# Kernel optimization log

Measured on AMD Instinct MI355X. Metric: run time of the kernel, lower is better.

## Reference

```python
import jax, jax.numpy as jnp
import numpy as np

EOS_IDX = 1
B, S, V, E, H = 32, 64, 32000, 512, 512


def _gru_step(x, h, w_ih, w_hh, b_ih, b_hh):
    # PyTorch GRU cell: gates ordered (r, z, n)
    gi = x @ w_ih.T + b_ih
    gh = h @ w_hh.T + b_hh
    i_r, i_z, i_n = jnp.split(gi, 3, axis=-1)
    h_r, h_z, h_n = jnp.split(gh, 3, axis=-1)
    r = jax.nn.sigmoid(i_r + h_r)
    z = jax.nn.sigmoid(i_z + h_z)
    n = jnp.tanh(i_n + r * h_n)
    return (1.0 - z) * n + z * h


def setup_inputs() -> dict:
    key = jax.random.key(0)
    ks = jax.random.split(key, 16)
    u = lambda k, shape: jax.random.uniform(k, shape, jnp.float32, -1.0, 1.0) / np.sqrt(H)
    return {
        "targets": jax.random.randint(ks[0], (B, S), 0, V),
        "targets_kws": jax.random.randint(ks[1], (B, S), 0, V),
        "sent_state": jax.random.normal(ks[2], (1, B, H), jnp.float32),
        "targets_len": jax.random.randint(ks[3], (B,), 1, S),
        "emb": jax.random.normal(ks[4], (V, E), jnp.float32) * 0.05,
        "w_ih_w": u(ks[5], (3 * H, 2 * E)),
        "w_hh_w": u(ks[6], (3 * H, H)),
        "b_ih_w": u(ks[7], (3 * H,)),
        "b_hh_w": u(ks[8], (3 * H,)),
        "w_ih_s": u(ks[9], (3 * H, H)),
        "w_hh_s": u(ks[10], (3 * H, H)),
        "b_ih_s": u(ks[11], (3 * H,)),
        "b_hh_s": u(ks[12], (3 * H,)),
        "out_w": u(ks[13], (V, H)),
        "out_b": u(ks[14], (V,)),
    }


def reference(targets, targets_kws, sent_state, targets_len,
              emb, w_ih_w, w_hh_w, b_ih_w, b_hh_w,
              w_ih_s, w_hh_s, b_ih_s, b_hh_s, out_w, out_b):
    seq = targets.shape[1]
    h0 = sent_state[0]  # nlayers = 1 -> (B, H)
    last_words = targets[:, :-1].T   # (S-1, B)
    keywords = targets_kws[:, 1:].T  # (S-1, B)
    next_words = targets[:, 1:].T    # (S-1, B)

    def step(carry, inp):
        word_h, sent_h = carry
        lw, kw, nw = inp
        x = jnp.concatenate([emb[kw], emb[lw]], axis=-1)  # (B, 2E)
        word_h = _gru_step(x, word_h, w_ih_w, w_hh_w, b_ih_w, b_hh_w)
        logp = jax.nn.log_softmax(word_h @ out_w.T + out_b, axis=-1)
        m = (nw == EOS_IDX).astype(word_h.dtype)[:, None]  # EOS mask
        tmp = _gru_step(word_h, sent_h, w_ih_s, w_hh_s, b_ih_s, b_hh_s)
        sent_h2 = sent_h * (1.0 - m) + tmp * m
        word_h2 = word_h * (1.0 - m) + tmp * m
        return (word_h2, sent_h2), logp

    _, logps = jax.lax.scan(step, (h0, h0), (last_words, keywords, next_words))
    # logps: (S-1, B, V). Masked NLL as in mask_loss().
    tok_logp = jnp.take_along_axis(logps, next_words[:, :, None], axis=2)[:, :, 0]
    valid = (targets_len[None, :] > jnp.arange(1, seq)[:, None]).astype(logps.dtype)
    return -(tok_logp * valid).sum()
```

## Files before the change

kernel.cpp:

```cpp
#include <hip/hip_runtime.h>
#include <stdint.h>

typedef short bf16x8 __attribute__((ext_vector_type(8)));
typedef float f32x4 __attribute__((ext_vector_type(4)));
typedef unsigned short u16;
typedef unsigned long long u64;

#define B_  32
#define S_  64
#define V_  32000
#define H_  512
#define T_  63
#define R_  2016
#define RP_ 2048
#define G3_ 1536
#define NWG 32
#define NWORK 192

#define o_X      0ull
#define o_Wih    4194304ull
#define o_OutW   7340032ull
#define o_PackHH 40108032ull
#define o_PackIS 41680896ull
#define o_PackHS 43253760ull
#define o_GI     44826624ull
#define o_WHf    57212928ull
#define o_WHb    61341696ull
#define o_HPUB   63438848ull
#define o_SPUB   63504384ull
#define o_ARR    63569920ull
#define o_CTR    63571968ull
#define o_PART   63733760ull
#define o_LSE    72122368ull
#define o_RL     72130560ull
#define o_FLG    72138752ull
#define o_HFLG   72139776ull

__device__ __forceinline__ u16 f2b(float f) {
  unsigned u = __float_as_uint(f);
  u = (u + 0x7FFFu + ((u >> 16) & 1u)) >> 16;
  return (u16)u;
}
__device__ __forceinline__ float sigm(float x) { return 1.0f / (1.0f + __expf(-x)); }

__device__ __forceinline__ void fbar(int* arr, int ph, int tid) {
  __syncthreads();
  if (tid == 0) {
    __hip_atomic_fetch_add(&arr[ph], 1, __ATOMIC_RELAXED, __HIP_MEMORY_SCOPE_AGENT);
    while (__hip_atomic_load(&arr[ph], __ATOMIC_RELAXED, __HIP_MEMORY_SCOPE_AGENT) < NWG)
      __builtin_amdgcn_s_sleep(1);
  }
  __syncthreads();
}

__global__ __launch_bounds__(256) void k_cvt(const float* __restrict__ src,
                                             u16* __restrict__ dst, int n) {
  int i4 = (blockIdx.x * 256 + threadIdx.x) * 4;
  if (i4 < n) {
    float4 v = *(const float4*)(src + i4);
    u16 t[4] = {f2b(v.x), f2b(v.y), f2b(v.z), f2b(v.w)};
    *(uint2*)(dst + i4) = *(uint2*)t;
  }
}

__global__ __launch_bounds__(256) void k_pack(const float* __restrict__ w, u16* __restrict__ up) {
  int uid = blockIdx.x * 256 + threadIdx.x;
  int lane = uid & 63;
  int ksct = uid >> 6;
  int ks = ksct & 15, ct = ksct >> 4;
  int nrow = ct * 16 + (lane & 15);
  int k0 = ks * 32 + (lane >> 4) * 8;
  const float* p = w + (size_t)nrow * 512 + k0;
  float4 v0 = *(const float4*)p;
  float4 v1 = *(const float4*)(p + 4);
  u16 t[8] = {f2b(v0.x), f2b(v0.y), f2b(v0.z), f2b(v0.w),
              f2b(v1.x), f2b(v1.y), f2b(v1.z), f2b(v1.w)};
  *(uint4*)(up + (size_t)uid * 8) = *(uint4*)t;
}

__global__ __launch_bounds__(256) void k_gather(const float* __restrict__ emb,
                                                const int* __restrict__ tg,
                                                const int* __restrict__ tk,
                                                u16* __restrict__ X) {
  int r = blockIdx.x;
  int tid = threadIdx.x;
  u16* xr = X + (size_t)r * 1024;
  if (r < R_) {
    int t = r >> 5, b = r & 31;
    int kw = tk[b * 64 + t + 1];
    int lw = tg[b * 64 + t];
    const float* src = (tid < 128) ? (emb + (size_t)kw * 512 + tid * 4)
                                   : (emb + (size_t)lw * 512 + (tid - 128) * 4);
    float4 v = *(const float4*)src;
    u16 o[4] = {f2b(v.x), f2b(v.y), f2b(v.z), f2b(v.w)};
    *(uint2*)(xr + tid * 4) = *(uint2*)o;
  } else {
    u16 z[4] = {0, 0, 0, 0};
    *(uint2*)(xr + tid * 4) = *(uint2*)z;
  }
}

__global__ __launch_bounds__(256) void k_init(const float* __restrict__ sent,
                                              const int* __restrict__ tg,
                                              u64* __restrict__ hpub, u64* __restrict__ spub,
                                              u16* __restrict__ whb, int* __restrict__ flg,
                                              int* __restrict__ arr, int* __restrict__ ctr,
                                              int* __restrict__ hflg) {
  int idx = blockIdx.x * 256 + threadIdx.x;
  whb[(size_t)R_ * 512 + idx] = 0;
  if (idx < 2048) {
    int b = idx >> 6, c = idx & 63;
    const float* p = sent + (size_t)b * 512 + c * 8;
    float4 v0 = *(const float4*)p;
    float4 v1 = *(const float4*)(p + 4);
    u16 t[8] = {f2b(v0.x), f2b(v0.y), f2b(v0.z), f2b(v0.w),
                f2b(v1.x), f2b(v1.y), f2b(v1.z), f2b(v1.w)};
    int slot = c ^ (b & 7);
    u64* d = hpub + b * 128 + slot * 2;
    d[0] = ((const u64*)t)[0];
    d[1] = ((const u64*)t)[1];
    u64* s = spub + b * 128 + slot * 2;
    s[0] = ((const u64*)t)[0];
    s[1] = ((const u64*)t)[1];
  }
  if (blockIdx.x == 0 && threadIdx.x < 63) {
    int f = 0;
    for (int b = 0; b < 32; ++b) f |= (tg[b * 64 + threadIdx.x + 1] == 1);
    flg[threadIdx.x] = f;
  }
  if (blockIdx.x == 1) arr[threadIdx.x] = 0;
  if (blockIdx.x == 2) ctr[threadIdx.x] = 0;
  if (blockIdx.x == 3) hflg[threadIdx.x] = 0;
  if (blockIdx.x == 4) hflg[256 + threadIdx.x] = 0;
}

__global__ __launch_bounds__(256) void k_gemm0(const u16* __restrict__ A, const u16* __restrict__ Bw,
                                               const float* __restrict__ bias, int N, int K, int nrt,
                                               float* __restrict__ outC, int Mstore) {
  __shared__ u16 As[128 * 64];
  __shared__ u16 Bs[128 * 64];
  int bid = blockIdx.x;
  int rt = bid % nrt, ct = bid / nrt;
  int m0 = rt * 128, n0 = ct * 128;
  int tid = threadIdx.x;
  int lane = tid & 63, wid = tid >> 6;
  int wr = wid >> 1, wc = wid & 1;
  f32x4 z = {0.f, 0.f, 0.f, 0.f};
  f32x4 acc[4][4];
#pragma unroll
  for (int i = 0; i < 4; ++i)
#pragma unroll
    for (int j = 0; j < 4; ++j) acc[i][j] = z;

  int nkt = K >> 6;
  for (int kt = 0; kt < nkt; ++kt) {
    __syncthreads();
#pragma unroll
    for (int it = 0; it < 4; ++it) {
      int idx = it * 256 + tid;
      int row = idx >> 3;
      int kch = idx & 7;
      int sch = kch ^ (row & 7);
      *(uint4*)(&As[row * 64 + kch * 8]) =
          *(const uint4*)(A + (size_t)(m0 + row) * K + kt * 64 + sch * 8);
      *(uint4*)(&Bs[row * 64 + kch * 8]) =
          *(const uint4*)(Bw + (size_t)(n0 + row) * K + kt * 64 + sch * 8);
    }
    __syncthreads();
#pragma unroll
    for (int kk = 0; kk < 2; ++kk) {
      bf16x8 af[4], bf[4];
#pragma unroll
      for (int i = 0; i < 4; ++i) {
        int row = wr * 64 + i * 16 + (lane & 15);
        int c = kk * 4 + (lane >> 4);
        af[i] = *(const bf16x8*)(&As[row * 64 + ((c ^ (row & 7)) * 8)]);
      }
#pragma unroll
      for (int j = 0; j < 4; ++j) {
        int row = wc * 64 + j * 16 + (lane & 15);
        int c = kk * 4 + (lane >> 4);
        bf[j] = *(const bf16x8*)(&Bs[row * 64 + ((c ^ (row & 7)) * 8)]);
      }
#pragma unroll
      for (int i = 0; i < 4; ++i)
#pragma unroll
        for (int j = 0; j < 4; ++j)
          acc[i][j] = __builtin_amdgcn_mfma_f32_16x16x32_bf16(af[i], bf[j], acc[i][j], 0, 0, 0);
    }
  }
#pragma unroll
  for (int i = 0; i < 4; ++i) {
    int mb = m0 + wr * 64 + i * 16 + ((lane >> 4) << 2);
#pragma unroll
    for (int j = 0; j < 4; ++j) {
      int n = n0 + wc * 64 + j * 16 + (lane & 15);
      float bb = bias[n];
#pragma unroll
      for (int r = 0; r < 4; ++r) {
        int m = mb + r;
        if (m < Mstore) outC[(size_t)m * N + n] = acc[i][j][r] + bb;
      }
    }
  }
}

struct RecurSM {
  u16 hb[32 * 512];
  u16 wls[3 * 1024 * 8];
  float ghl[6][32][16];
  float gil[2][3][32][16];
  float hloc[32][16];
  float sloc[32][16];
  u16 hps[32][16];
  u16 sps[32][16];
};
struct GemmSM {
  u16 As[128 * 64];
  u16 Bs[128 * 64];
};
union MegaSM {
  RecurSM r;
  GemmSM g;
};

__device__ __forceinline__ f32x4 mm16_lds(const u16* hb, const u16* bl, int lane, int rt) {
  f32x4 a0 = {0.f, 0.f, 0.f, 0.f}, a1 = {0.f, 0.f, 0.f, 0.f};
  int row = rt * 16 + (lane & 15);
  int cb = lane >> 4;
#pragma unroll
  for (int ks = 0; ks < 16; ks += 2) {
    int c0 = ks * 4 + cb, c1 = c0 + 4;
    bf16x8 av0 = *(const bf16x8*)(&hb[row * 512 + ((c0 ^ (row & 7)) * 8)]);
    bf16x8 bv0 = *(const bf16x8*)(&bl[(ks * 64 + lane) * 8]);
    bf16x8 av1 = *(const bf16x8*)(&hb[row * 512 + ((c1 ^ (row & 7)) * 8)]);
    bf16x8 bv1 = *(const bf16x8*)(&bl[((ks + 1) * 64 + lane) * 8]);
    a0 = __builtin_amdgcn_mfma_f32_16x16x32_bf16(av0, bv0, a0, 0, 0, 0);
    a1 = __builtin_amdgcn_mfma_f32_16x16x32_bf16(av1, bv1, a1, 0, 0, 0);
  }
  return a0 + a1;
}

__device__ __forceinline__ f32x4 mm16g(const u16* hb, const u16* bp, int lane, int rt) {
  f32x4 acc = {0.f, 0.f, 0.f, 0.f};
#pragma unroll
  for (int ks = 0; ks < 16; ++ks) {
    int row = rt * 16 + (lane & 15);
    int c = ks * 4 + (lane >> 4);
    bf16x8 a = *(const bf16x8*)(&hb[row * 512 + ((c ^ (row & 7)) * 8)]);
    bf16x8 b = *(const bf16x8*)(bp + (size_t)(ks * 64 + lane) * 8);
    acc = __builtin_amdgcn_mfma_f32_16x16x32_bf16(a, b, acc, 0, 0, 0);
  }
  return acc;
}

__device__ __forceinline__ void gemm_tile(u16* As, u16* Bs, const u16* __restrict__ A,
                                          const u16* __restrict__ Bw,
                                          const float* __restrict__ bias,
                                          int rt, int ct, float2* __restrict__ parts, int tid) {
  int m0 = rt * 128, n0 = ct * 128;
  int lane = tid & 63, wid = tid >> 6;
  int wr = wid >> 1, wc = wid & 1;
  f32x4 z = {0.f, 0.f, 0.f, 0.f};
  f32x4 acc[2][4];
#pragma unroll
  for (int i = 0; i < 2; ++i)
#pragma unroll
    for (int j = 0; j < 4; ++j) acc[i][j] = z;

  for (int kt = 0; kt < 8; ++kt) {
    __syncthreads();
#pragma unroll
    for (int it = 0; it < 2; ++it) {
      int idx = it * 512 + tid;
      int row = idx >> 3, kch = idx & 7;
      *(uint4*)(&As[row * 64 + kch * 8]) =
          *(const uint4*)(A + (size_t)(m0 + row) * 512 + kt * 64 + kch * 8);
      int sch = kch ^ (row & 7);
      *(uint4*)(&Bs[row * 64 + kch * 8]) =
          *(const uint4*)(Bw + (size_t)(n0 + row) * 512 + kt * 64 + sch * 8);
    }
    __syncthreads();
#pragma unroll
    for (int kk = 0; kk < 2; ++kk) {
      bf16x8 af[2], bf[4];
#pragma unroll
      for (int i = 0; i < 2; ++i) {
        int row = wr * 32 + i * 16 + (lane & 15);
        int c = kk * 4 + (lane >> 4);
        af[i] = *(const bf16x8*)(&As[row * 64 + ((c ^ (row & 7)) * 8)]);
      }
#pragma unroll
      for (int j = 0; j < 4; ++j) {
        int row = wc * 64 + j * 16 + (lane & 15);
        int c = kk * 4 + (lane >> 4);
        bf[j] = *(const bf16x8*)(&Bs[row * 64 + ((c ^ (row & 7)) * 8)]);
      }
#pragma unroll
      for (int i = 0; i < 2; ++i)
#pragma unroll
        for (int j = 0; j < 4; ++j)
          acc[i][j] = __builtin_amdgcn_mfma_f32_16x16x32_bf16(af[i], bf[j], acc[i][j], 0, 0, 0);
    }
  }
  float bb[4];
#pragma unroll
  for (int j = 0; j < 4; ++j) bb[j] = bias[n0 + wc * 64 + j * 16 + (lane & 15)];
  int chunk = ct * 2 + wc;
#pragma unroll
  for (int i = 0; i < 2; ++i) {
#pragma unroll
    for (int r = 0; r < 4; ++r) {
      float l0 = acc[i][0][r] + bb[0], l1 = acc[i][1][r] + bb[1];
      float l2 = acc[i][2][r] + bb[2], l3 = acc[i][3][r] + bb[3];
      float mx = fmaxf(fmaxf(l0, l1), fmaxf(l2, l3));
#pragma unroll
      for (int d = 1; d < 16; d <<= 1) mx = fmaxf(mx, __shfl_xor(mx, d));
      float s = __expf(l0 - mx) + __expf(l1 - mx) + __expf(l2 - mx) + __expf(l3 - mx);
#pragma unroll
      for (int d = 1; d < 16; d <<= 1) s += __shfl_xor(s, d);
      if ((lane & 15) == 0) {
        int m = m0 + wr * 32 + i * 16 + ((lane >> 4) << 2) + r;
        parts[(size_t)m * 512 + chunk] = make_float2(mx, s);
      }
    }
  }
}

__global__ __launch_bounds__(512) void k_mega(
    const float* __restrict__ gi, const u16* __restrict__ packHH, const u16* __restrict__ packIS,
    const u16* __restrict__ packHS, const float* __restrict__ bhh_w, const float* __restrict__ bih_s,
    const float* __restrict__ bhh_s, const int* __restrict__ targets, const int* __restrict__ flags,
    const float* __restrict__ sent, u64* __restrict__ hpub, u64* __restrict__ spub,
    float* __restrict__ whf, u16* __restrict__ whb, int* __restrict__ arr, int* __restrict__ ctr,
    int* __restrict__ hflg, u16* __restrict__ outw16, const float* __restrict__ outw,
    const float* __restrict__ outb, float2* __restrict__ parts) {
  __shared__ MegaSM sm;
  const int tid = threadIdx.x;
  int* steps = ctr + 32;

  if (blockIdx.x >= NWG) {
    const int w = blockIdx.x - NWG;
    const int nown = (w < 58) ? 2 : 1;
#pragma unroll
    for (int p = 0; p < 2; ++p) {
      if (p < nown) {
        int ct = w + p * 192;
        const float* src = outw + (size_t)ct * 65536;
        u16* dst = outw16 + (size_t)ct * 65536;
        for (int it = 0; it < 32; ++it) {
          int e = it * 512 + tid;
          float4 v = *(const float4*)(src + (size_t)e * 4);
          u16 t[4] = {f2b(v.x), f2b(v.y), f2b(v.z), f2b(v.w)};
          *(uint2*)(dst + (size_t)e * 4) = *(uint2*)t;
        }
      }
    }
    __syncthreads();
    for (int rt = 0; rt < 16; ++rt) {
      if (tid == 0) {
        int need = 4 * rt + 4;
        if (need > T_) need = T_;
        while (__hip_atomic_load(steps, __ATOMIC_RELAXED, __HIP_MEMORY_SCOPE_AGENT) < need)
          __builtin_amdgcn_s_sleep(64);
        (void)__hip_atomic_load(steps, __ATOMIC_ACQUIRE, __HIP_MEMORY_SCOPE_AGENT);
      }
      for (int p = 0; p < nown; ++p)
        gemm_tile(sm.g.As, sm.g.Bs, whb, outw16, outb, rt, w + p * 192, parts, tid);
      __syncthreads();
    }
    return;
  }

  const int lane = tid & 63;
  const int wid = tid >> 6;
  const int gate = wid >> 1;
  const int rt = wid & 1;
  const int g = blockIdx.x;
  const int b_ = tid >> 4, hl = tid & 15;
  const int n_ = g * 16 + hl;

  {
    const uint4* src = (const uint4*)packHH;
    uint4* dst = (uint4*)sm.r.wls;
    for (int lin = tid; lin < 3072; lin += 512) {
      int which = lin >> 10, off = lin & 1023;
      dst[lin] = src[(size_t)(which * 32 + g) * 1024 + off];
    }
  }
  {
    float v = sent[(size_t)b_ * 512 + n_];
    sm.r.hloc[b_][hl] = v;
    sm.r.sloc[b_][hl] = v;
  }
  if (wid >= 6) {
    int lid = tid - 384;
    const float* base = gi + (size_t)g * 16;
#pragma unroll
    for (int q = 0; q < 3; ++q) {
      int fid = q * 128 + lid;
      int ga = fid >> 7, rem = fid & 127;
      int b = rem >> 2, h4 = (rem & 3) << 2;
      *(float4*)&sm.r.gil[0][ga][b][h4] = *(const float4*)(base + (size_t)b * 1536 + ga * 512 + h4);
    }
  }
  const float bw_r = bhh_w[n_], bw_z = bhh_w[512 + n_], bw_n = bhh_w[1024 + n_];
  __syncthreads();

  int ph = 0;
  int scur = 0;
  for (int t = 0; t < T_; ++t) {
    const int cur = t & 1, nxt = cur ^ 1;
    if (wid == 0) {
      for (;;) {
        int f = (lane < 32)
            ? __hip_atomic_load(&hflg[lane * 16], __ATOMIC_RELAXED, __HIP_MEMORY_SCOPE_AGENT)
            : 0x7fffffff;
        if (__all(f >= t)) break;
        __builtin_amdgcn_s_sleep(1);
      }
      if (g == 0 && lane == 0)
        __hip_atomic_store(steps, t, __ATOMIC_RELEASE, __HIP_MEMORY_SCOPE_AGENT);
    }
    __syncthreads();
    {
      const u64* src = hpub + cur * 4096;
      u64* d = (u64*)sm.r.hb;
      for (int idx = tid; idx < 4096; idx += 512)
        d[idx] = __hip_atomic_load(&src[idx], __ATOMIC_RELAXED, __HIP_MEMORY_SCOPE_AGENT);
    }
    __syncthreads();
    if (wid < 6) {
      f32x4 acc = mm16_lds(sm.r.hb, sm.r.wls + gate * 8192, lane, rt);
      int bb = rt * 16 + ((lane >> 4) << 2);
      int cl = lane & 15;
#pragma unroll
      for (int r4 = 0; r4 < 4; ++r4) sm.r.ghl[gate][bb + r4][cl] = acc[r4];
    } else if (t + 1 < T_) {
      int lid = tid - 384;
      const float* base = gi + (size_t)(t + 1) * 32 * 1536 + g * 16;
#pragma unroll
      for (int q = 0; q < 3; ++q) {
        int fid = q * 128 + lid;
        int ga = fid >> 7, rem = fid & 127;
        int b = rem >> 2, h4 = (rem & 3) << 2;
        *(float4*)&sm.r.gil[nxt][ga][b][h4] =
            *(const float4*)(base + (size_t)b * 1536 + ga * 512 + h4);
      }
    }
    __syncthreads();
    {
      int rrow = t * 32 + b_;
      float r_ = sigm(sm.r.gil[cur][0][b_][hl] + sm.r.ghl[0][b_][hl] + bw_r);
      float z_ = sigm(sm.r.gil[cur][1][b_][hl] + sm.r.ghl[1][b_][hl] + bw_z);
      float nn = tanhf(sm.r.gil[cur][2][b_][hl] + r_ * (sm.r.ghl[2][b_][hl] + bw_n));
      float hold = sm.r.hloc[b_][hl];
      float hnew = (1.f - z_) * nn + z_ * hold;
      sm.r.hloc[b_][hl] = hnew;
      sm.r.hps[b_][hl] = f2b(hnew);
      whf[(size_t)rrow * 512 + n_] = hnew;
    }
    __syncthreads();
    if (tid < 128) {
      int b = tid >> 2, j = tid & 3, q = j >> 1, half = j & 1;
      u64 v = *(const u64*)&sm.r.hps[b][q * 8 + half * 4];
      int slot = (2 * g + q) ^ (b & 7);
      __hip_atomic_store(&hpub[nxt * 4096 + b * 128 + slot * 2 + half], v,
                         __ATOMIC_RELAXED, __HIP_MEMORY_SCOPE_AGENT);
    } else if (tid < 256) {
      int l = tid - 128;
      int b = l >> 2, j = l & 3, q = j >> 1, half = j & 1;
      u64 v = *(const u64*)&sm.r.hps[b][q * 8 + half * 4];
      int slot = (2 * g + q) ^ (b & 7);
      __hip_atomic_store((u64*)whb + (size_t)(t * 32 + b) * 128 + slot * 2 + half, v,
                         __ATOMIC_RELAXED, __HIP_MEMORY_SCOPE_AGENT);
    }

    if (!flags[t]) {
      __syncthreads();
      if (tid == 0)
        __hip_atomic_store(&hflg[g * 16], t + 1, __ATOMIC_RELAXED, __HIP_MEMORY_SCOPE_AGENT);
    } else {
      fbar(arr, ph, tid); ++ph;
      {
        const u64* src = hpub + nxt * 4096;
        u64* d = (u64*)sm.r.hb;
        for (int idx = tid; idx < 4096; idx += 512)
          d[idx] = __hip_atomic_load(&src[idx], __ATOMIC_RELAXED, __HIP_MEMORY_SCOPE_AGENT);
      }
      fbar(arr, ph, tid); ++ph;
      f32x4 ax = {0.f, 0.f, 0.f, 0.f};
      if (wid < 6) ax = mm16g(sm.r.hb, packIS + (size_t)(gate * 32 + g) * 8192, lane, rt);
      __syncthreads();
      {
        const u64* src = spub + scur * 4096;
        u64* d = (u64*)sm.r.hb;
        for (int idx = tid; idx < 4096; idx += 512)
          d[idx] = __hip_atomic_load(&src[idx], __ATOMIC_RELAXED, __HIP_MEMORY_SCOPE_AGENT);
      }
      __syncthreads();
      if (wid < 6) {
        f32x4 ah = mm16g(sm.r.hb, packHS + (size_t)(gate * 32 + g) * 8192, lane, rt);
        int bb = rt * 16 + ((lane >> 4) << 2);
        int cl = lane & 15;
#pragma unroll
        for (int r4 = 0; r4 < 4; ++r4) {
          sm.r.ghl[gate][bb + r4][cl] = ax[r4];
          sm.r.ghl[3 + gate][bb + r4][cl] = ah[r4];
        }
      }
      __syncthreads();
      {
        float r_ = sigm(sm.r.ghl[0][b_][hl] + bih_s[n_] + sm.r.ghl[3][b_][hl] + bhh_s[n_]);
        float z_ = sigm(sm.r.ghl[1][b_][hl] + bih_s[512 + n_] + sm.r.ghl[4][b_][hl] + bhh_s[512 + n_]);
        float nn = tanhf(sm.r.ghl[2][b_][hl] + bih_s[1024 + n_] +
                         r_ * (sm.r.ghl[5][b_][hl] + bhh_s[1024 + n_]));
        float hs = sm.r.sloc[b_][hl];
        float tmpv = (1.f - z_) * nn + z_ * hs;
        int m = (targets[b_ * 64 + t + 1] == 1);
        float hw = sm.r.hloc[b_][hl];
        float hw2 = m ? tmpv : hw;
        float hs2 = m ? tmpv : hs;
        sm.r.hloc[b_][hl] = hw2;
        sm.r.sloc[b_][hl] = hs2;
        sm.r.hps[b_][hl] = f2b(hw2);
        sm.r.sps[b_][hl] = f2b(hs2);
      }
      __syncthreads();
      if (tid < 128) {
        int b = tid >> 2, j = tid & 3, q = j >> 1, half = j & 1;
        int slot = (2 * g + q) ^ (b & 7);
        u64 v = *(const u64*)&sm.r.hps[b][q * 8 + half * 4];
        __hip_atomic_store(&hpub[nxt * 4096 + b * 128 + slot * 2 + half], v,
                           __ATOMIC_RELAXED, __HIP_MEMORY_SCOPE_AGENT);
        u64 w2 = *(const u64*)&sm.r.sps[b][q * 8 + half * 4];
        __hip_atomic_store(&spub[(scur ^ 1) * 4096 + b * 128 + slot * 2 + half], w2,
                           __ATOMIC_RELAXED, __HIP_MEMORY_SCOPE_AGENT);
      }
      scur ^= 1;
      __syncthreads();
      if (tid == 0)
        __hip_atomic_store(&hflg[g * 16], t + 1, __ATOMIC_RELAXED, __HIP_MEMORY_SCOPE_AGENT);
    }
  }
  if (g == 0 && wid == 0) {
    for (;;) {
      int f = (lane < 32)
          ? __hip_atomic_load(&hflg[lane * 16], __ATOMIC_RELAXED, __HIP_MEMORY_SCOPE_AGENT)
          : 0x7fffffff;
      if (__all(f >= T_)) break;
      __builtin_amdgcn_s_sleep(1);
    }
    if (lane == 0)
      __hip_atomic_store(steps, T_, __ATOMIC_RELEASE, __HIP_MEMORY_SCOPE_AGENT);
  }
}

__global__ __launch_bounds__(256) void k_lse(const float2* __restrict__ parts,
                                             float* __restrict__ lse) {
  int wid = threadIdx.x >> 6, lane = threadIdx.x & 63;
  int row = blockIdx.x * 4 + wid;
  if (row >= R_) return;
  float m = -3.0e38f, s = 0.f;
  for (int c = lane; c < 500; c += 64) {
    float2 p = parts[(size_t)row * 512 + c];
    float nm = fmaxf(m, p.x);
    s = s * __expf(m - nm) + p.y * __expf(p.x - nm);
    m = nm;
  }
#pragma unroll
  for (int d = 1; d < 64; d <<= 1) {
    float om = __shfl_xor(m, d), os = __shfl_xor(s, d);
    float nm = fmaxf(m, om);
    s = s * __expf(m - nm) + os * __expf(om - nm);
    m = nm;
  }
  if (lane == 0) lse[row] = m + __logf(s);
}

__global__ __launch_bounds__(256) void k_rowloss(const float* __restrict__ whf,
                                                 const float* __restrict__ outw,
                                                 const float* __restrict__ outb,
                                                 const int* __restrict__ targets,
                                                 const int* __restrict__ tlen,
                                                 const float* __restrict__ lse,
                                                 float* __restrict__ rl) {
  int wid = threadIdx.x >> 6, lane = threadIdx.x & 63;
  int r = blockIdx.x * 4 + wid;
  if (r >= R_) return;
  int t = r >> 5, b = r & 31;
  int nw = targets[b * 64 + t + 1];
  const float* hv = whf + (size_t)r * 512;
  const float* wv = outw + (size_t)nw * 512;
  float acc = 0.f;
#pragma unroll
  for (int q = 0; q < 2; ++q) {
    int k = lane * 8 + q * 4;
    float4 a = *(const float4*)(hv + k);
    float4 w = *(const float4*)(wv + k);
    acc += a.x * w.x + a.y * w.y + a.z * w.z + a.w * w.w;
  }
#pragma unroll
  for (int d = 1; d < 64; d <<= 1) acc += __shfl_xor(acc, d);
  if (lane == 0) {
    bool valid = tlen[b] > (t + 1);
    rl[r] = valid ? (lse[r] - (acc + outb[nw])) : 0.f;
  }
}

__global__ __launch_bounds__(256) void k_sum(const float* __restrict__ rl, float* __restrict__ out) {
  __shared__ float sm[256];
  float a = 0.f;
  for (int i = threadIdx.x; i < R_; i += 256) a += rl[i];
  sm[threadIdx.x] = a;
  __syncthreads();
  for (int s = 128; s > 0; s >>= 1) {
    if (threadIdx.x < s) sm[threadIdx.x] += sm[threadIdx.x + s];
    __syncthreads();
  }
  if (threadIdx.x == 0) out[0] = sm[0];
}

extern "C" void kernel_launch(void* const* d_in, const int* in_sizes, int n_in,
                              void* d_out, int out_size, void* d_ws, size_t ws_size,
                              hipStream_t stream) {
  const int* targets = (const int*)d_in[0];
  const int* tkws    = (const int*)d_in[1];
  const float* sent  = (const float*)d_in[2];
  const int* tlen    = (const int*)d_in[3];
  const float* emb   = (const float*)d_in[4];
  const float* wihw  = (const float*)d_in[5];
  const float* whhw  = (const float*)d_in[6];
  const float* bihw  = (const float*)d_in[7];
  const float* bhhw  = (const float*)d_in[8];
  const float* wihs  = (const float*)d_in[9];
  const float* whhs  = (const float*)d_in[10];
  const float* bihs  = (const float*)d_in[11];
  const float* bhhs  = (const float*)d_in[12];
  const float* outw  = (const float*)d_in[13];
  const float* outb  = (const float*)d_in[14];
  float* out = (float*)d_out;
  char* ws = (char*)d_ws;

  u16* X       = (u16*)(ws + o_X);
  u16* Wih16   = (u16*)(ws + o_Wih);
  u16* OutW16  = (u16*)(ws + o_OutW);
  u16* PackHH  = (u16*)(ws + o_PackHH);
  u16* PackIS  = (u16*)(ws + o_PackIS);
  u16* PackHS  = (u16*)(ws + o_PackHS);
  float* GI    = (float*)(ws + o_GI);
  float* WHf   = (float*)(ws + o_WHf);
  u16* WHb     = (u16*)(ws + o_WHb);
  u64* HPUB    = (u64*)(ws + o_HPUB);
  u64* SPUB    = (u64*)(ws + o_SPUB);
  int* ARR     = (int*)(ws + o_ARR);
  int* CTR     = (int*)(ws + o_CTR);
  float2* PART = (float2*)(ws + o_PART);
  float* LSE   = (float*)(ws + o_LSE);
  float* RL    = (float*)(ws + o_RL);
  int* FLG     = (int*)(ws + o_FLG);
  int* HFLG    = (int*)(ws + o_HFLG);

  k_cvt<<<dim3(1536), dim3(256), 0, stream>>>(wihw, Wih16, G3_ * 1024);
  k_pack<<<dim3(384), dim3(256), 0, stream>>>(whhw, PackHH);
  k_pack<<<dim3(384), dim3(256), 0, stream>>>(wihs, PackIS);
  k_pack<<<dim3(384), dim3(256), 0, stream>>>(whhs, PackHS);
  k_gather<<<dim3(RP_), dim3(256), 0, stream>>>(emb, targets, tkws, X);
  k_init<<<dim3(64), dim3(256), 0, stream>>>(sent, targets, HPUB, SPUB, WHb, FLG, ARR, CTR, HFLG);

  k_gemm0<<<dim3(16 * 12), dim3(256), 0, stream>>>(X, Wih16, bihw, G3_, 1024, 16, GI, R_);

  k_mega<<<dim3(NWG + NWORK), dim3(512), 0, stream>>>(GI, PackHH, PackIS, PackHS, bhhw, bihs, bhhs,
                                                      targets, FLG, sent, HPUB, SPUB, WHf, WHb,
                                                      ARR, CTR, HFLG, OutW16, outw, outb, PART);

  k_lse<<<dim3(504), dim3(256), 0, stream>>>(PART, LSE);
  k_rowloss<<<dim3(504), dim3(256), 0, stream>>>(WHf, outw, outb, targets, tlen, LSE, RL);
  k_sum<<<dim3(1), dim3(256), 0, stream>>>(RL, out);
}
```

Before: 393.6 us.

## Fuse prep kernels into one launch, fuse LSE/rowloss/sum, shrink worker grid

Merges the six preprocessing kernels (convert, three packs, gather, init) into a single k_prep launch dispatched by block index. It also merges the log-sum-exp, row-loss and final-sum kernels into one k_final that reduces per timestep and adds into the output with atomicAdd. The output is zeroed in k_prep. Separately, the number of output-GEMM worker blocks in the persistent kernel drops from 192 to 128, so more workers own two column tiles. This cuts launch overhead and intermediate buffers, but the smaller worker count may lengthen the logits GEMM tail, and the float atomic sum makes the result order-dependent.

```diff
diff --git a/kernel.cpp b/kernel.cpp
--- a/kernel.cpp
+++ b/kernel.cpp
@@ -15,7 +15,7 @@
 #define RP_ 2048
 #define G3_ 1536
 #define NWG 32
-#define NWORK 192
+#define NWORK 128
 
 #define o_X      0ull
 #define o_Wih    4194304ull
@@ -53,85 +53,89 @@
   __syncthreads();
 }
 
-__global__ __launch_bounds__(256) void k_cvt(const float* __restrict__ src,
-                                             u16* __restrict__ dst, int n) {
-  int i4 = (blockIdx.x * 256 + threadIdx.x) * 4;
-  if (i4 < n) {
-    float4 v = *(const float4*)(src + i4);
-    u16 t[4] = {f2b(v.x), f2b(v.y), f2b(v.z), f2b(v.w)};
-    *(uint2*)(dst + i4) = *(uint2*)t;
-  }
-}
-
-__global__ __launch_bounds__(256) void k_pack(const float* __restrict__ w, u16* __restrict__ up) {
-  int uid = blockIdx.x * 256 + threadIdx.x;
-  int lane = uid & 63;
-  int ksct = uid >> 6;
-  int ks = ksct & 15, ct = ksct >> 4;
-  int nrow = ct * 16 + (lane & 15);
-  int k0 = ks * 32 + (lane >> 4) * 8;
-  const float* p = w + (size_t)nrow * 512 + k0;
-  float4 v0 = *(const float4*)p;
-  float4 v1 = *(const float4*)(p + 4);
-  u16 t[8] = {f2b(v0.x), f2b(v0.y), f2b(v0.z), f2b(v0.w),
-              f2b(v1.x), f2b(v1.y), f2b(v1.z), f2b(v1.w)};
-  *(uint4*)(up + (size_t)uid * 8) = *(uint4*)t;
-}
-
-__global__ __launch_bounds__(256) void k_gather(const float* __restrict__ emb,
-                                                const int* __restrict__ tg,
-                                                const int* __restrict__ tk,
-                                                u16* __restrict__ X) {
-  int r = blockIdx.x;
-  int tid = threadIdx.x;
-  u16* xr = X + (size_t)r * 1024;
-  if (r < R_) {
-    int t = r >> 5, b = r & 31;
-    int kw = tk[b * 64 + t + 1];
-    int lw = tg[b * 64 + t];
-    const float* src = (tid < 128) ? (emb + (size_t)kw * 512 + tid * 4)
-                                   : (emb + (size_t)lw * 512 + (tid - 128) * 4);
-    float4 v = *(const float4*)src;
-    u16 o[4] = {f2b(v.x), f2b(v.y), f2b(v.z), f2b(v.w)};
-    *(uint2*)(xr + tid * 4) = *(uint2*)o;
+__global__ __launch_bounds__(256) void k_prep(
+    const float* __restrict__ emb, const int* __restrict__ tg, const int* __restrict__ tk,
+    u16* __restrict__ X, const float* __restrict__ sent, u64* __restrict__ hpub,
+    u64* __restrict__ spub, u16* __restrict__ whb, int* __restrict__ flg, int* __restrict__ arr,
+    int* __restrict__ ctr, int* __restrict__ hflg, const float* __restrict__ wihw,
+    u16* __restrict__ wih16, const float* __restrict__ whhw, u16* __restrict__ packHH,
+    const float* __restrict__ wihs, u16* __restrict__ packIS, const float* __restrict__ whhs,
+    u16* __restrict__ packHS, float* __restrict__ out) {
+  const int bid = blockIdx.x;
+  const int tid = threadIdx.x;
+  if (bid < 2048) {
+    int r = bid;
+    u16* xr = X + (size_t)r * 1024;
+    if (r < R_) {
+      int t = r >> 5, b = r & 31;
+      int kw = tk[b * 64 + t + 1];
+      int lw = tg[b * 64 + t];
+      const float* src = (tid < 128) ? (emb + (size_t)kw * 512 + tid * 4)
+                                     : (emb + (size_t)lw * 512 + (tid - 128) * 4);
+      float4 v = *(const float4*)src;
+      u16 o[4] = {f2b(v.x), f2b(v.y), f2b(v.z), f2b(v.w)};
+      *(uint2*)(xr + tid * 4) = *(uint2*)o;
+    } else {
+      u16 z[4] = {0, 0, 0, 0};
+      *(uint2*)(xr + tid * 4) = *(uint2*)z;
+    }
+  } else if (bid < 2112) {
+    int lb = bid - 2048;
+    int idx = lb * 256 + tid;
+    whb[(size_t)R_ * 512 + idx] = 0;
+    if (idx < 2048) {
+      int b = idx >> 6, c = idx & 63;
+      const float* p = sent + (size_t)b * 512 + c * 8;
+      float4 v0 = *(const float4*)p;
+      float4 v1 = *(const float4*)(p + 4);
+      u16 t[8] = {f2b(v0.x), f2b(v0.y), f2b(v0.z), f2b(v0.w),
+                  f2b(v1.x), f2b(v1.y), f2b(v1.z), f2b(v1.w)};
+      int slot = c ^ (b & 7);
+      u64* d = hpub + b * 128 + slot * 2;
+      d[0] = ((const u64*)t)[0];
+      d[1] = ((const u64*)t)[1];
+      u64* s = spub + b * 128 + slot * 2;
+      s[0] = ((const u64*)t)[0];
+      s[1] = ((const u64*)t)[1];
+    }
+    if (lb == 0 && tid < 63) {
+      int f = 0;
+      for (int b = 0; b < 32; ++b) f |= (tg[b * 64 + tid + 1] == 1);
+      flg[tid] = f;
+    }
+    if (lb == 1) arr[tid] = 0;
+    if (lb == 2) ctr[tid] = 0;
+    if (lb == 3) hflg[tid] = 0;
+    if (lb == 4) hflg[256 + tid] = 0;
+    if (lb == 5 && tid == 0) out[0] = 0.f;
+  } else if (bid < 3648) {
+    int i4 = ((bid - 2112) * 256 + tid) * 4;
+    if (i4 < G3_ * 1024) {
+      float4 v = *(const float4*)(wihw + i4);
+      u16 t[4] = {f2b(v.x), f2b(v.y), f2b(v.z), f2b(v.w)};
+      *(uint2*)(wih16 + i4) = *(uint2*)t;
+    }
   } else {
-    u16 z[4] = {0, 0, 0, 0};
-    *(uint2*)(xr + tid * 4) = *(uint2*)z;
-  }
-}
-
-__global__ __launch_bounds__(256) void k_init(const float* __restrict__ sent,
-                                              const int* __restrict__ tg,
-                                              u64* __restrict__ hpub, u64* __restrict__ spub,
-                                              u16* __restrict__ whb, int* __restrict__ flg,
-                                              int* __restrict__ arr, int* __restrict__ ctr,
-                                              int* __restrict__ hflg) {
-  int idx = blockIdx.x * 256 + threadIdx.x;
-  whb[(size_t)R_ * 512 + idx] = 0;
-  if (idx < 2048) {
-    int b = idx >> 6, c = idx & 63;
-    const float* p = sent + (size_t)b * 512 + c * 8;
+    int pb = bid - 3648;
+    const float* w;
+    u16* up;
+    int lb;
+    if (pb < 384) { w = whhw; up = packHH; lb = pb; }
+    else if (pb < 768) { w = wihs; up = packIS; lb = pb - 384; }
+    else { w = whhs; up = packHS; lb = pb - 768; }
+    int uid = lb * 256 + tid;
+    int lane = uid & 63;
+    int ksct = uid >> 6;
+    int ks = ksct & 15, ct = ksct >> 4;
+    int nrow = ct * 16 + (lane & 15);
+    int k0 = ks * 32 + (lane >> 4) * 8;
+    const float* p = w + (size_t)nrow * 512 + k0;
     float4 v0 = *(const float4*)p;
     float4 v1 = *(const float4*)(p + 4);
     u16 t[8] = {f2b(v0.x), f2b(v0.y), f2b(v0.z), f2b(v0.w),
                 f2b(v1.x), f2b(v1.y), f2b(v1.z), f2b(v1.w)};
-    int slot = c ^ (b & 7);
-    u64* d = hpub + b * 128 + slot * 2;
-    d[0] = ((const u64*)t)[0];
-    d[1] = ((const u64*)t)[1];
-    u64* s = spub + b * 128 + slot * 2;
-    s[0] = ((const u64*)t)[0];
-    s[1] = ((const u64*)t)[1];
-  }
-  if (blockIdx.x == 0 && threadIdx.x < 63) {
-    int f = 0;
-    for (int b = 0; b < 32; ++b) f |= (tg[b * 64 + threadIdx.x + 1] == 1);
-    flg[threadIdx.x] = f;
-  }
-  if (blockIdx.x == 1) arr[threadIdx.x] = 0;
-  if (blockIdx.x == 2) ctr[threadIdx.x] = 0;
-  if (blockIdx.x == 3) hflg[threadIdx.x] = 0;
-  if (blockIdx.x == 4) hflg[256 + threadIdx.x] = 0;
+    *(uint4*)(up + (size_t)uid * 8) = *(uint4*)t;
+  }
 }
 
 __global__ __launch_bounds__(256) void k_gemm0(const u16* __restrict__ A, const u16* __restrict__ Bw,
@@ -341,11 +345,11 @@
 
   if (blockIdx.x >= NWG) {
     const int w = blockIdx.x - NWG;
-    const int nown = (w < 58) ? 2 : 1;
+    const int nown = (w < 122) ? 2 : 1;
 #pragma unroll
     for (int p = 0; p < 2; ++p) {
       if (p < nown) {
-        int ct = w + p * 192;
+        int ct = w + p * NWORK;
         const float* src = outw + (size_t)ct * 65536;
         u16* dst = outw16 + (size_t)ct * 65536;
         for (int it = 0; it < 32; ++it) {
@@ -366,7 +370,7 @@
         (void)__hip_atomic_load(steps, __ATOMIC_ACQUIRE, __HIP_MEMORY_SCOPE_AGENT);
       }
       for (int p = 0; p < nown; ++p)
-        gemm_tile(sm.g.As, sm.g.Bs, whb, outw16, outb, rt, w + p * 192, parts, tid);
+        gemm_tile(sm.g.As, sm.g.Bs, whb, outw16, outb, rt, w + p * NWORK, parts, tid);
       __syncthreads();
     }
     return;
@@ -556,69 +560,62 @@
   }
 }
 
-__global__ __launch_bounds__(256) void k_lse(const float2* __restrict__ parts,
-                                             float* __restrict__ lse) {
-  int wid = threadIdx.x >> 6, lane = threadIdx.x & 63;
-  int row = blockIdx.x * 4 + wid;
-  if (row >= R_) return;
-  float m = -3.0e38f, s = 0.f;
-  for (int c = lane; c < 500; c += 64) {
-    float2 p = parts[(size_t)row * 512 + c];
-    float nm = fmaxf(m, p.x);
-    s = s * __expf(m - nm) + p.y * __expf(p.x - nm);
-    m = nm;
-  }
-#pragma unroll
-  for (int d = 1; d < 64; d <<= 1) {
-    float om = __shfl_xor(m, d), os = __shfl_xor(s, d);
-    float nm = fmaxf(m, om);
-    s = s * __expf(m - nm) + os * __expf(om - nm);
-    m = nm;
-  }
-  if (lane == 0) lse[row] = m + __logf(s);
-}
-
-__global__ __launch_bounds__(256) void k_rowloss(const float* __restrict__ whf,
-                                                 const float* __restrict__ outw,
-                                                 const float* __restrict__ outb,
-                                                 const int* __restrict__ targets,
-                                                 const int* __restrict__ tlen,
-                                                 const float* __restrict__ lse,
-                                                 float* __restrict__ rl) {
-  int wid = threadIdx.x >> 6, lane = threadIdx.x & 63;
-  int r = blockIdx.x * 4 + wid;
-  if (r >= R_) return;
-  int t = r >> 5, b = r & 31;
-  int nw = targets[b * 64 + t + 1];
-  const float* hv = whf + (size_t)r * 512;
-  const float* wv = outw + (size_t)nw * 512;
-  float acc = 0.f;
-#pragma unroll
-  for (int q = 0; q < 2; ++q) {
-    int k = lane * 8 + q * 4;
-    float4 a = *(const float4*)(hv + k);
-    float4 w = *(const float4*)(wv + k);
-    acc += a.x * w.x + a.y * w.y + a.z * w.z + a.w * w.w;
-  }
-#pragma unroll
-  for (int d = 1; d < 64; d <<= 1) acc += __shfl_xor(acc, d);
-  if (lane == 0) {
-    bool valid = tlen[b] > (t + 1);
-    rl[r] = valid ? (lse[r] - (acc + outb[nw])) : 0.f;
-  }
-}
-
-__global__ __launch_bounds__(256) void k_sum(const float* __restrict__ rl, float* __restrict__ out) {
-  __shared__ float sm[256];
-  float a = 0.f;
-  for (int i = threadIdx.x; i < R_; i += 256) a += rl[i];
-  sm[threadIdx.x] = a;
+__global__ __launch_bounds__(512) void k_final(const float2* __restrict__ parts,
+                                               const float* __restrict__ whf,
+                                               const float* __restrict__ outw,
+                                               const float* __restrict__ outb,
+                                               const int* __restrict__ targets,
+                                               const int* __restrict__ tlen,
+                                               float* __restrict__ out) {
+  const int t = blockIdx.x;
+  const int tid = threadIdx.x;
+  const int wv = tid >> 6, lane = tid & 63;
+  __shared__ float wsum[8];
+  float lsum = 0.f;
+#pragma unroll
+  for (int q = 0; q < 4; ++q) {
+    int b = wv * 4 + q;
+    int r = t * 32 + b;
+    float m = -3.0e38f, s = 0.f;
+    for (int c = lane; c < 500; c += 64) {
+      float2 p = parts[(size_t)r * 512 + c];
+      float nm = fmaxf(m, p.x);
+      s = s * __expf(m - nm) + p.y * __expf(p.x - nm);
+      m = nm;
+    }
+#pragma unroll
+    for (int d = 1; d < 64; d <<= 1) {
+      float om = __shfl_xor(m, d), os = __shfl_xor(s, d);
+      float nm = fmaxf(m, om);
+      s = s * __expf(m - nm) + os * __expf(om - nm);
+      m = nm;
+    }
+    float lse = m + __logf(s);
+    int nw = targets[b * 64 + t + 1];
+    const float* hv = whf + (size_t)r * 512;
+    const float* wvp = outw + (size_t)nw * 512;
+    int k = lane * 8;
+    float4 a0 = *(const float4*)(hv + k);
+    float4 w0 = *(const float4*)(wvp + k);
+    float4 a1 = *(const float4*)(hv + k + 4);
+    float4 w1 = *(const float4*)(wvp + k + 4);
+    float acc = a0.x * w0.x + a0.y * w0.y + a0.z * w0.z + a0.w * w0.w +
+                a1.x * w1.x + a1.y * w1.y + a1.z * w1.z + a1.w * w1.w;
+#pragma unroll
+    for (int d = 1; d < 64; d <<= 1) acc += __shfl_xor(acc, d);
+    if (lane == 0) {
+      bool valid = tlen[b] > (t + 1);
+      lsum += valid ? (lse - (acc + outb[nw])) : 0.f;
+    }
+  }
+  if (lane == 0) wsum[wv] = lsum;
   __syncthreads();
-  for (int s = 128; s > 0; s >>= 1) {
-    if (threadIdx.x < s) sm[threadIdx.x] += sm[threadIdx.x + s];
-    __syncthreads();
-  }
-  if (threadIdx.x == 0) out[0] = sm[0];
+  if (tid == 0) {
+    float a = 0.f;
+#pragma unroll
+    for (int i = 0; i < 8; ++i) a += wsum[i];
+    atomicAdd(out, a);
+  }
 }
 
 extern "C" void kernel_launch(void* const* d_in, const int* in_sizes, int n_in,
@@ -656,17 +653,12 @@
   int* ARR     = (int*)(ws + o_ARR);
   int* CTR     = (int*)(ws + o_CTR);
   float2* PART = (float2*)(ws + o_PART);
-  float* LSE   = (float*)(ws + o_LSE);
-  float* RL    = (float*)(ws + o_RL);
   int* FLG     = (int*)(ws + o_FLG);
   int* HFLG    = (int*)(ws + o_HFLG);
 
-  k_cvt<<<dim3(1536), dim3(256), 0, stream>>>(wihw, Wih16, G3_ * 1024);
-  k_pack<<<dim3(384), dim3(256), 0, stream>>>(whhw, PackHH);
-  k_pack<<<dim3(384), dim3(256), 0, stream>>>(wihs, PackIS);
-  k_pack<<<dim3(384), dim3(256), 0, stream>>>(whhs, PackHS);
-  k_gather<<<dim3(RP_), dim3(256), 0, stream>>>(emb, targets, tkws, X);
-  k_init<<<dim3(64), dim3(256), 0, stream>>>(sent, targets, HPUB, SPUB, WHb, FLG, ARR, CTR, HFLG);
+  k_prep<<<dim3(4800), dim3(256), 0, stream>>>(emb, targets, tkws, X, sent, HPUB, SPUB, WHb,
+                                               FLG, ARR, CTR, HFLG, wihw, Wih16,
+                                               whhw, PackHH, wihs, PackIS, whhs, PackHS, out);
 
   k_gemm0<<<dim3(16 * 12), dim3(256), 0, stream>>>(X, Wih16, bihw, G3_, 1024, 16, GI, R_);
 
@@ -674,7 +666,5 @@
                                                       targets, FLG, sent, HPUB, SPUB, WHf, WHb,
                                                       ARR, CTR, HFLG, OutW16, outw, outb, PART);
 
-  k_lse<<<dim3(504), dim3(256), 0, stream>>>(PART, LSE);
-  k_rowloss<<<dim3(504), dim3(256), 0, stream>>>(WHf, outw, outb, targets, tlen, LSE, RL);
-  k_sum<<<dim3(1), dim3(256), 0, stream>>>(RL, out);
-}
+  k_final<<<dim3(T_), dim3(512), 0, stream>>>(PART, WHf, outw, outb, targets, tlen, out);
+}
```

Result: no change. 401.3 us (+2.0%).
